# Performance work log

Hardware: AMD Instinct MI355X
Metric: run time of the kernel (lower is better)

The kernel has to match this reference:

```python
import jax, jax.numpy as jnp
import numpy as np

C = 8.0  # RG-LRU temporal-gate constant (Griffin paper, c = 8)


def setup_inputs() -> dict:
    key = jax.random.key(0)
    ks = jax.random.split(key, 4)
    S, B, D = 2048, 8, 2048  # (seq_len, batch, width); batch_first=False layout
    s = 1.0 / np.sqrt(D).astype(np.float32)
    return {
        "x": jax.random.normal(ks[0], (S, B, D), jnp.float32),
        "h0": jnp.zeros((B, D), jnp.float32),
        "W_x": jax.random.normal(ks[1], (D, D), jnp.float32) * s,
        "b_x": jnp.zeros((D,), jnp.float32),
        "W_a": jax.random.normal(ks[2], (D, D), jnp.float32) * s,
        "b_a": jnp.zeros((D,), jnp.float32),
        "a_param": jax.random.uniform(ks[3], (D,), jnp.float32, 0.3, 1.0),
    }


def _rg_lru(x, h0, W_x, b_x, W_a, b_a, a_param):
    # x: (S, B, D) time-major. RG-LRU (Griffin/Hawk), num_heads=1 so the
    # block-diagonal gate projections are plain dense D->D linears.
    S = x.shape[0]
    gate_x = jax.nn.sigmoid(jnp.einsum("sbd,ed->sbe", x, W_x) + b_x)  # input gate
    gate_a = jax.nn.sigmoid(jnp.einsum("sbd,ed->sbe", x, W_a) + b_a)  # recurrence gate
    log_a = -C * gate_a * jax.nn.softplus(a_param)  # (S, B, D), log of decay in (0,1)
    a = jnp.exp(log_a)
    multiplier = jnp.sqrt(1.0 - jnp.exp(2.0 * log_a))  # sqrt(1 - a^2) normalizer
    # Reset at segment start (t == 0): multiplier -> 1, decay -> 0 (cache cleared).
    reset = (jnp.arange(S) == 0)[:, None, None]
    multiplier = jnp.where(reset, 1.0, multiplier)
    a = jnp.where(reset, 0.0, a)
    normed_x = x * gate_x * multiplier  # gated, variance-normalized input

    def step(h, inp):
        a_t, x_t = inp
        h = a_t * h + x_t  # diagonal linear recurrence
        return h, h

    hn, y = jax.lax.scan(step, h0, (a, normed_x))
    return y, hn  # y: (S, B, D) since batch_first=False; hn: (B, D)


def reference(x, h0, W_x, b_x, W_a, b_a, a_param):
    return _rg_lru(x, h0, W_x, b_x, W_a, b_a, a_param)
```

## Files before the change

kernel.cpp:

```cpp
#include <hip/hip_runtime.h>
#include <cstdint>

#define S_LEN 2048
#define B_SZ 8
#define D_DIM 2048
#define M_DIM (S_LEN * B_SZ)
#define CHAINS (B_SZ * D_DIM)
#define BK 64
#define KTILES (D_DIM / BK)

typedef __bf16 bf16;
typedef bf16 bf16x8 __attribute__((ext_vector_type(8)));
typedef bf16 bf16x4 __attribute__((ext_vector_type(4)));
typedef float f32x4 __attribute__((ext_vector_type(4)));

__device__ __forceinline__ void async_copy16(void* lds, const void* g) {
    __builtin_amdgcn_global_load_lds(
        (const __attribute__((address_space(1))) unsigned int*)g,
        (__attribute__((address_space(3))) unsigned int*)lds,
        16, 0, 0);
}

__device__ __forceinline__ unsigned short bf16_bits(float f) {
    bf16 b = (bf16)f;
    return __builtin_bit_cast(unsigned short, b);
}

__global__ void k_convert(const float4* __restrict__ x,
                          const float4* __restrict__ wx,
                          const float4* __restrict__ wa,
                          bf16* __restrict__ xb,
                          bf16* __restrict__ wi) {
    const long NX4 = (long)M_DIM * D_DIM / 4;
    const long NW4 = (long)D_DIM * D_DIM / 4;
    const long total = NX4 + 2 * NW4;
    for (long i = (long)blockIdx.x * blockDim.x + threadIdx.x; i < total;
         i += (long)gridDim.x * blockDim.x) {
        float4 v;
        bf16* dst;
        if (i < NX4) {
            v = x[i];
            dst = xb + 4 * i;
        } else {
            long k = i - NX4;
            const int isA = k >= NW4;
            if (isA) k -= NW4;
            const long e = k >> 9;
            const long col4 = k & 511;
            const long drow = (e >> 4) * 32 + (isA ? 16 : 0) + (e & 15);
            v = (isA ? wa : wx)[k];
            dst = wi + (drow * 512 + col4) * 4;
        }
        bf16x4 o;
        o[0] = (bf16)v.x; o[1] = (bf16)v.y; o[2] = (bf16)v.z; o[3] = (bf16)v.w;
        *reinterpret_cast<bf16x4*>(dst) = o;
    }
}

__global__ void k_cvec(const float* __restrict__ ap, float* __restrict__ cv) {
    int e = blockIdx.x * blockDim.x + threadIdx.x;
    if (e < D_DIM) {
        float v = ap[e];
        cv[e] = -8.0f * log1pf(expf(v));
    }
}

__global__ __launch_bounds__(512, 2) void k_gemm(
    const bf16* __restrict__ xb,
    const bf16* __restrict__ wi,
    const float* __restrict__ bx,
    const float* __restrict__ ba,
    const float* __restrict__ cv,
    unsigned int* __restrict__ pk)
{
    __shared__ __align__(16) char smem[131072];

    const int tid  = threadIdx.x;
    const int lane = tid & 63;
    const int w    = tid >> 6;
    const int wm   = w >> 2;
    const int wn   = w & 3;

    const int orig = blockIdx.x;
    const int wgid = (orig & 7) * 128 + (orig >> 3);
    const int m0 = (wgid & 63) * 256;
    const int e0 = (wgid >> 6) * 256;

    const int srow  = lane >> 3;
    const int swz16 = ((lane & 7) ^ srow) * 16;

    const char* gA = (const char*)xb;
    const char* gB = (const char*)wi;

#define SU_A(buf, kt, u) do {                                                  \
    const int rb_ = (u) * 64 + w * 8;                                          \
    async_copy16(smem + (buf) * 65536 + rb_ * 128,                             \
                 gA + ((long)(m0 + rb_ + srow) * 4096 +                        \
                       (long)(kt) * 128 + swz16));                             \
    } while (0)

#define SU_B(buf, kt, u) do {                                                  \
    const int rb_ = (u) * 64 + w * 8;                                          \
    async_copy16(smem + (buf) * 65536 + 32768 + rb_ * 128,                     \
                 gB + ((long)(e0 + rb_ + srow) * 4096 +                        \
                       (long)(kt) * 128 + swz16));                             \
    } while (0)

    f32x4 acc[8][4];
#pragma unroll
    for (int i = 0; i < 8; ++i)
#pragma unroll
        for (int j = 0; j < 4; ++j) acc[i][j] = (f32x4)(0.0f);

    SU_A(0, 0, 0); SU_A(0, 0, 2);
    SU_B(0, 0, 0); SU_B(0, 0, 1); SU_B(0, 0, 2); SU_B(0, 0, 3);
    SU_A(0, 0, 1); SU_A(0, 0, 3);
    asm volatile("s_waitcnt vmcnt(2)" ::: "memory");
    __builtin_amdgcn_s_barrier();

    const int rL = lane & 15;

    for (int kt = 0; kt < KTILES; ++kt) {
        const int c  = kt & 1;
        const int nb = 1 - c;
        char* sA = smem + c * 65536;
        char* sB = sA + 32768;
        const bool pf = (kt < KTILES - 1);

        bf16x8 af[4], bf[4];

#define LOAD_AF(ihalf, ks) do {                                                \
    _Pragma("unroll")                                                          \
    for (int i_ = 0; i_ < 4; ++i_) {                                           \
        const int r_ = wm * 128 + ((ihalf) * 4 + i_) * 16 + rL;                \
        const int ch_ = (((ks) * 4 + (lane >> 4)) ^ (r_ & 7)) * 16;            \
        af[i_] = *reinterpret_cast<const bf16x8*>(sA + r_ * 128 + ch_);        \
    } } while (0)

#define LOAD_BF(ks) do {                                                       \
    _Pragma("unroll")                                                          \
    for (int j_ = 0; j_ < 4; ++j_) {                                           \
        const int r_ = wn * 64 + j_ * 16 + rL;                                 \
        const int ch_ = (((ks) * 4 + (lane >> 4)) ^ (r_ & 7)) * 16;            \
        bf[j_] = *reinterpret_cast<const bf16x8*>(sB + r_ * 128 + ch_);        \
    } } while (0)

#define MFMA16(ihalf) do {                                                     \
    _Pragma("unroll")                                                          \
    for (int i_ = 0; i_ < 4; ++i_)                                             \
        _Pragma("unroll")                                                      \
        for (int j_ = 0; j_ < 4; ++j_)                                         \
            acc[(ihalf) * 4 + i_][j_] = __builtin_amdgcn_mfma_f32_16x16x32_bf16( \
                af[i_], bf[j_], acc[(ihalf) * 4 + i_][j_], 0, 0, 0);           \
    } while (0)

        LOAD_BF(0); LOAD_AF(0, 0);
        if (pf) { SU_A(nb, kt + 1, 0); SU_A(nb, kt + 1, 2); }
        MFMA16(0);
        if (pf) asm volatile("s_waitcnt vmcnt(2)" ::: "memory");
        else    asm volatile("s_waitcnt vmcnt(0)" ::: "memory");
        __builtin_amdgcn_s_barrier();

        LOAD_AF(1, 0);
        if (pf) { SU_B(nb, kt + 1, 0); SU_B(nb, kt + 1, 1); }
        MFMA16(1);

        LOAD_BF(1); LOAD_AF(0, 1);
        if (pf) { SU_B(nb, kt + 1, 2); SU_B(nb, kt + 1, 3); }
        MFMA16(0);

        LOAD_AF(1, 1);
        if (pf) { SU_A(nb, kt + 1, 1); SU_A(nb, kt + 1, 3); }
        MFMA16(1);

        if (pf) {
            asm volatile("s_waitcnt vmcnt(2)" ::: "memory");
            __builtin_amdgcn_s_barrier();
        }

#undef LOAD_AF
#undef LOAD_BF
#undef MFMA16
    }

#undef SU_A
#undef SU_B

    const int rgrp = lane >> 4;
    const int chb  = (e0 + wn * 64) >> 1;
#pragma unroll
    for (int jj = 0; jj < 2; ++jj) {
        const int ch = chb + jj * 16 + rL;
        const float bxv = bx[ch];
        const float bav = ba[ch];
        const float cvv = cv[ch];
#pragma unroll
        for (int i = 0; i < 8; ++i) {
#pragma unroll
            for (int r = 0; r < 4; ++r) {
                const int m = m0 + wm * 128 + i * 16 + rgrp * 4 + r;
                const float zx = acc[i][2 * jj][r] + bxv;
                const float za = acc[i][2 * jj + 1][r] + bav;
                const float gx = 1.0f / (1.0f + __expf(-zx));
                const float ga = 1.0f / (1.0f + __expf(-za));
                float la = cvv * ga;
                float mult = sqrtf(fmaxf(1.0f - __expf(2.0f * la), 0.0f));
                if (m < B_SZ) { la = -100.0f; mult = 1.0f; }
                const long o = (long)m * D_DIM + ch;
                const float xv = (float)xb[o];
                const float xn = xv * gx * mult;
                const unsigned int u =
                    ((unsigned int)bf16_bits(xn) << 16) | bf16_bits(la);
                pk[o] = u;
            }
        }
    }
}

__global__ __launch_bounds__(64) void k_scan(
    const unsigned int* __restrict__ pk,
    float* __restrict__ y,
    const float* __restrict__ h0,
    float* __restrict__ hn) {
    const int c = blockIdx.x * 64 + threadIdx.x;
    float h = h0[c];

    unsigned int u0[16], u1[16];
#pragma unroll
    for (int j = 0; j < 16; ++j) u0[j] = pk[(long)j * CHAINS + c];

    for (int g = 0; g < 128; g += 2) {
        const long base1 = ((long)(g + 1) * 16) * CHAINS + c;
        if (g + 1 < 128) {
#pragma unroll
            for (int j = 0; j < 16; ++j) u1[j] = pk[base1 + (long)j * CHAINS];
        }
        const long base0 = ((long)g * 16) * CHAINS + c;
#pragma unroll
        for (int j = 0; j < 16; ++j) {
            const unsigned int u = u0[j];
            const float la = __builtin_bit_cast(float, u << 16);
            const float xn = __builtin_bit_cast(float, u & 0xffff0000u);
            h = fmaf(__expf(la), h, xn);
            y[base0 + (long)j * CHAINS] = h;
        }
        const long base2 = ((long)(g + 2) * 16) * CHAINS + c;
        if (g + 2 < 128) {
#pragma unroll
            for (int j = 0; j < 16; ++j) u0[j] = pk[base2 + (long)j * CHAINS];
        }
        if (g + 1 < 128) {
#pragma unroll
            for (int j = 0; j < 16; ++j) {
                const unsigned int u = u1[j];
                const float la = __builtin_bit_cast(float, u << 16);
                const float xn = __builtin_bit_cast(float, u & 0xffff0000u);
                h = fmaf(__expf(la), h, xn);
                y[base1 + (long)j * CHAINS] = h;
            }
        }
    }
    hn[c] = h;
}

extern "C" void kernel_launch(void* const* d_in, const int* in_sizes, int n_in,
                              void* d_out, int out_size, void* d_ws, size_t ws_size,
                              hipStream_t stream) {
    const float* x  = (const float*)d_in[0];
    const float* h0 = (const float*)d_in[1];
    const float* Wx = (const float*)d_in[2];
    const float* bx = (const float*)d_in[3];
    const float* Wa = (const float*)d_in[4];
    const float* ba = (const float*)d_in[5];
    const float* ap = (const float*)d_in[6];
    float* out = (float*)d_out;

    char* ws = (char*)d_ws;
    bf16*  xb = (bf16*)(ws);
    bf16*  wi = (bf16*)(ws + 67108864L);
    float* cv = (float*)(ws + 83886080L);
    unsigned int* pk = (unsigned int*)(ws + 83894272L);

    float* y  = out;
    float* hn = out + (long)M_DIM * D_DIM;

    k_convert<<<dim3(2048), dim3(256), 0, stream>>>(
        (const float4*)x, (const float4*)Wx, (const float4*)Wa, xb, wi);
    k_cvec<<<dim3(8), dim3(256), 0, stream>>>(ap, cv);
    k_gemm<<<dim3((M_DIM / 256) * (2 * D_DIM / 256)), dim3(512), 0, stream>>>(
        xb, wi, bx, ba, cv, pk);
    k_scan<<<dim3(CHAINS / 64), dim3(64), 0, stream>>>(pk, y, h0, hn);
}
```

Measured before the change: 428.2 us.

## Restructure GEMM main loop into quadrant phases with barriers and s_setprio

```diff
diff --git a/kernel.cpp b/kernel.cpp
--- a/kernel.cpp
+++ b/kernel.cpp
@@ -106,16 +106,25 @@
                        (long)(kt) * 128 + swz16));                             \
     } while (0)
 
+#define PHASE_MID() do {                                                       \
+    __builtin_amdgcn_s_barrier();                                              \
+    asm volatile("s_waitcnt lgkmcnt(0)" ::: "memory");                         \
+    __builtin_amdgcn_sched_barrier(0);                                         \
+    __builtin_amdgcn_s_setprio(1); } while (0)
+
+#define PHASE_END() do {                                                       \
+    __builtin_amdgcn_s_setprio(0);                                             \
+    __builtin_amdgcn_s_barrier(); } while (0)
+
     f32x4 acc[8][4];
 #pragma unroll
     for (int i = 0; i < 8; ++i)
 #pragma unroll
         for (int j = 0; j < 4; ++j) acc[i][j] = (f32x4)(0.0f);
 
-    SU_A(0, 0, 0); SU_A(0, 0, 2);
+    SU_A(0, 0, 0); SU_A(0, 0, 1); SU_A(0, 0, 2); SU_A(0, 0, 3);
     SU_B(0, 0, 0); SU_B(0, 0, 1); SU_B(0, 0, 2); SU_B(0, 0, 3);
-    SU_A(0, 0, 1); SU_A(0, 0, 3);
-    asm volatile("s_waitcnt vmcnt(2)" ::: "memory");
+    asm volatile("s_waitcnt vmcnt(0)" ::: "memory");
     __builtin_amdgcn_s_barrier();
 
     const int rL = lane & 15;
@@ -127,64 +136,74 @@
         char* sB = sA + 32768;
         const bool pf = (kt < KTILES - 1);
 
-        bf16x8 af[4], bf[4];
-
-#define LOAD_AF(ihalf, ks) do {                                                \
-    _Pragma("unroll")                                                          \
-    for (int i_ = 0; i_ < 4; ++i_) {                                           \
-        const int r_ = wm * 128 + ((ihalf) * 4 + i_) * 16 + rL;                \
-        const int ch_ = (((ks) * 4 + (lane >> 4)) ^ (r_ & 7)) * 16;            \
-        af[i_] = *reinterpret_cast<const bf16x8*>(sA + r_ * 128 + ch_);        \
-    } } while (0)
-
-#define LOAD_BF(ks) do {                                                       \
-    _Pragma("unroll")                                                          \
-    for (int j_ = 0; j_ < 4; ++j_) {                                           \
-        const int r_ = wn * 64 + j_ * 16 + rL;                                 \
-        const int ch_ = (((ks) * 4 + (lane >> 4)) ^ (r_ & 7)) * 16;            \
-        bf[j_] = *reinterpret_cast<const bf16x8*>(sB + r_ * 128 + ch_);        \
-    } } while (0)
-
-#define MFMA16(ihalf) do {                                                     \
+        bf16x8 a0[8], a1[8], b0[4], b1[4];
+
+#define READ_A(dst, sub) do {                                                  \
     _Pragma("unroll")                                                          \
     for (int i_ = 0; i_ < 4; ++i_)                                             \
         _Pragma("unroll")                                                      \
-        for (int j_ = 0; j_ < 4; ++j_)                                         \
-            acc[(ihalf) * 4 + i_][j_] = __builtin_amdgcn_mfma_f32_16x16x32_bf16( \
-                af[i_], bf[j_], acc[(ihalf) * 4 + i_][j_], 0, 0, 0);           \
+        for (int ks_ = 0; ks_ < 2; ++ks_) {                                    \
+            const int r_ = wm * 128 + (sub) * 64 + i_ * 16 + rL;               \
+            const int ch_ = ((ks_ * 4 + (lane >> 4)) ^ (r_ & 7)) * 16;         \
+            dst[i_ * 2 + ks_] =                                                \
+                *reinterpret_cast<const bf16x8*>(sA + r_ * 128 + ch_);         \
+        } } while (0)
+
+#define READ_B(dst, sub) do {                                                  \
+    _Pragma("unroll")                                                          \
+    for (int j_ = 0; j_ < 2; ++j_)                                             \
+        _Pragma("unroll")                                                      \
+        for (int ks_ = 0; ks_ < 2; ++ks_) {                                    \
+            const int r_ = wn * 64 + (sub) * 32 + j_ * 16 + rL;                \
+            const int ch_ = ((ks_ * 4 + (lane >> 4)) ^ (r_ & 7)) * 16;         \
+            dst[j_ * 2 + ks_] =                                                \
+                *reinterpret_cast<const bf16x8*>(sB + r_ * 128 + ch_);         \
+        } } while (0)
+
+#define MFMAQ(ih, jh, am, bm) do {                                             \
+    _Pragma("unroll")                                                          \
+    for (int i_ = 0; i_ < 4; ++i_)                                             \
+        _Pragma("unroll")                                                      \
+        for (int j_ = 0; j_ < 2; ++j_)                                         \
+            _Pragma("unroll")                                                  \
+            for (int ks_ = 0; ks_ < 2; ++ks_)                                  \
+                acc[(ih) * 4 + i_][(jh) * 2 + j_] =                            \
+                    __builtin_amdgcn_mfma_f32_16x16x32_bf16(                   \
+                        am[i_ * 2 + ks_], bm[j_ * 2 + ks_],                    \
+                        acc[(ih) * 4 + i_][(jh) * 2 + j_], 0, 0, 0);           \
     } while (0)
 
-        LOAD_BF(0); LOAD_AF(0, 0);
-        if (pf) { SU_A(nb, kt + 1, 0); SU_A(nb, kt + 1, 2); }
-        MFMA16(0);
-        if (pf) asm volatile("s_waitcnt vmcnt(2)" ::: "memory");
-        else    asm volatile("s_waitcnt vmcnt(0)" ::: "memory");
+        READ_A(a0, 0); READ_B(b0, 0);
+        if (pf) { SU_A(nb, kt + 1, 0); SU_A(nb, kt + 1, 1);
+                  SU_A(nb, kt + 1, 2); SU_A(nb, kt + 1, 3); }
+        PHASE_MID();
+        MFMAQ(0, 0, a0, b0);
+        PHASE_END();
+
+        READ_B(b1, 1);
+        if (pf) { SU_B(nb, kt + 1, 0); SU_B(nb, kt + 1, 1);
+                  SU_B(nb, kt + 1, 2); SU_B(nb, kt + 1, 3); }
+        PHASE_MID();
+        MFMAQ(0, 1, a0, b1);
+        PHASE_END();
+
+        READ_A(a1, 1);
+        PHASE_MID();
+        MFMAQ(1, 1, a1, b1);
+        MFMAQ(1, 0, a1, b0);
+        __builtin_amdgcn_s_setprio(0);
+        if (pf) asm volatile("s_waitcnt vmcnt(0)" ::: "memory");
         __builtin_amdgcn_s_barrier();
 
-        LOAD_AF(1, 0);
-        if (pf) { SU_B(nb, kt + 1, 0); SU_B(nb, kt + 1, 1); }
-        MFMA16(1);
-
-        LOAD_BF(1); LOAD_AF(0, 1);
-        if (pf) { SU_B(nb, kt + 1, 2); SU_B(nb, kt + 1, 3); }
-        MFMA16(0);
-
-        LOAD_AF(1, 1);
-        if (pf) { SU_A(nb, kt + 1, 1); SU_A(nb, kt + 1, 3); }
-        MFMA16(1);
-
-        if (pf) {
-            asm volatile("s_waitcnt vmcnt(2)" ::: "memory");
-            __builtin_amdgcn_s_barrier();
-        }
-
-#undef LOAD_AF
-#undef LOAD_BF
-#undef MFMA16
+#undef READ_A
+#undef READ_B
+#undef MFMAQ
     }
 
 #undef SU_A
 #undef SU_B
+#undef PHASE_MID
+#undef PHASE_END
 
     const int rgrp = lane >> 4;
     const int chb  = (e0 + wn * 64) >> 1;
```

Result: no change. 427.3 us (-0.2%).

## Pre-swizzle weights into MFMA fragment order and load B directly to registers

Applied to the files above, without the earlier changes.

```diff
diff --git a/kernel.cpp b/kernel.cpp
--- a/kernel.cpp
+++ b/kernel.cpp
@@ -30,30 +30,39 @@
                           const float4* __restrict__ wx,
                           const float4* __restrict__ wa,
                           bf16* __restrict__ xb,
-                          bf16* __restrict__ wi) {
+                          bf16* __restrict__ wsw) {
     const long NX4 = (long)M_DIM * D_DIM / 4;
-    const long NW4 = (long)D_DIM * D_DIM / 4;
-    const long total = NX4 + 2 * NW4;
+    const long NWS = 1048576;
+    const long total = NX4 + NWS;
     for (long i = (long)blockIdx.x * blockDim.x + threadIdx.x; i < total;
          i += (long)gridDim.x * blockDim.x) {
-        float4 v;
-        bf16* dst;
         if (i < NX4) {
-            v = x[i];
-            dst = xb + 4 * i;
+            float4 v = x[i];
+            bf16x4 o;
+            o[0] = (bf16)v.x; o[1] = (bf16)v.y; o[2] = (bf16)v.z; o[3] = (bf16)v.w;
+            *reinterpret_cast<bf16x4*>(xb + 4 * i) = o;
         } else {
-            long k = i - NX4;
-            const int isA = k >= NW4;
-            if (isA) k -= NW4;
-            const long e = k >> 9;
-            const long col4 = k & 511;
-            const long drow = (e >> 4) * 32 + (isA ? 16 : 0) + (e & 15);
-            v = (isA ? wa : wx)[k];
-            dst = wi + (drow * 512 + col4) * 4;
-        }
-        bf16x4 o;
-        o[0] = (bf16)v.x; o[1] = (bf16)v.y; o[2] = (bf16)v.z; o[3] = (bf16)v.w;
-        *reinterpret_cast<bf16x4*>(dst) = o;
+            const long t = i - NX4;
+            const int lane = (int)(t & 63);
+            const long frag = t >> 6;
+            const int ks = (int)(frag & 1);
+            const int cg = (int)((frag >> 1) & 15);
+            const int kt = (int)((frag >> 5) & 31);
+            const int nb = (int)(frag >> 10);
+            const int lr = lane & 15, ch = lane >> 4;
+            const int g  = cg & 1;
+            const int e  = (((nb << 4) | cg) >> 1) * 16 + lr;
+            const int d  = kt * 64 + ks * 32 + ch * 8;
+            const float4* src = (g ? wa : wx) + (long)e * 512 + (d >> 2);
+            const float4 v0 = src[0];
+            const float4 v1 = src[1];
+            bf16x8 o;
+            o[0] = (bf16)v0.x; o[1] = (bf16)v0.y;
+            o[2] = (bf16)v0.z; o[3] = (bf16)v0.w;
+            o[4] = (bf16)v1.x; o[5] = (bf16)v1.y;
+            o[6] = (bf16)v1.z; o[7] = (bf16)v1.w;
+            *reinterpret_cast<bf16x8*>(wsw + t * 8) = o;
+        }
     }
 }
 
@@ -67,13 +76,13 @@
 
 __global__ __launch_bounds__(512, 2) void k_gemm(
     const bf16* __restrict__ xb,
-    const bf16* __restrict__ wi,
+    const bf16* __restrict__ wsw,
     const float* __restrict__ bx,
     const float* __restrict__ ba,
     const float* __restrict__ cv,
     unsigned int* __restrict__ pk)
 {
-    __shared__ __align__(16) char smem[131072];
+    __shared__ __align__(16) char smem[65536];
 
     const int tid  = threadIdx.x;
     const int lane = tid & 63;
@@ -83,51 +92,32 @@
 
     const int orig = blockIdx.x;
     const int wgid = (orig & 7) * 128 + (orig >> 3);
-    const int m0 = (wgid & 63) * 256;
-    const int e0 = (wgid >> 6) * 256;
+    const int m0  = (wgid & 63) * 256;
+    const int nbb = wgid >> 6;
+    const int e0  = nbb * 256;
 
     const int srow  = lane >> 3;
     const int swz16 = ((lane & 7) ^ srow) * 16;
+    const int rL = lane & 15;
 
     const char* gA = (const char*)xb;
-    const char* gB = (const char*)wi;
 
 #define SU_A(buf, kt, u) do {                                                  \
     const int rb_ = (u) * 64 + w * 8;                                          \
-    async_copy16(smem + (buf) * 65536 + rb_ * 128,                             \
+    async_copy16(smem + (buf) * 32768 + rb_ * 128,                             \
                  gA + ((long)(m0 + rb_ + srow) * 4096 +                        \
                        (long)(kt) * 128 + swz16));                             \
     } while (0)
 
-#define SU_B(buf, kt, u) do {                                                  \
-    const int rb_ = (u) * 64 + w * 8;                                          \
-    async_copy16(smem + (buf) * 65536 + 32768 + rb_ * 128,                     \
-                 gB + ((long)(e0 + rb_ + srow) * 4096 +                        \
-                       (long)(kt) * 128 + swz16));                             \
-    } while (0)
-
-    f32x4 acc[8][4];
-#pragma unroll
-    for (int i = 0; i < 8; ++i)
-#pragma unroll
-        for (int j = 0; j < 4; ++j) acc[i][j] = (f32x4)(0.0f);
-
-    SU_A(0, 0, 0); SU_A(0, 0, 2);
-    SU_B(0, 0, 0); SU_B(0, 0, 1); SU_B(0, 0, 2); SU_B(0, 0, 3);
-    SU_A(0, 0, 1); SU_A(0, 0, 3);
-    asm volatile("s_waitcnt vmcnt(2)" ::: "memory");
-    __builtin_amdgcn_s_barrier();
-
-    const int rL = lane & 15;
-
-    for (int kt = 0; kt < KTILES; ++kt) {
-        const int c  = kt & 1;
-        const int nb = 1 - c;
-        char* sA = smem + c * 65536;
-        char* sB = sA + 32768;
-        const bool pf = (kt < KTILES - 1);
-
-        bf16x8 af[4], bf[4];
+#define LOAD_BG(dst, kt) do {                                                  \
+    _Pragma("unroll")                                                          \
+    for (int j_ = 0; j_ < 4; ++j_)                                             \
+        _Pragma("unroll")                                                      \
+        for (int ks_ = 0; ks_ < 2; ++ks_)                                      \
+            dst[j_ * 2 + ks_] = *reinterpret_cast<const bf16x8*>(              \
+                wsw + ((((long)nbb * 32 + (kt)) * 32) +                        \
+                       (wn * 4 + j_) * 2 + ks_) * 512 + lane * 8);             \
+    } while (0)
 
 #define LOAD_AF(ihalf, ks) do {                                                \
     _Pragma("unroll")                                                          \
@@ -137,54 +127,62 @@
         af[i_] = *reinterpret_cast<const bf16x8*>(sA + r_ * 128 + ch_);        \
     } } while (0)
 
-#define LOAD_BF(ks) do {                                                       \
-    _Pragma("unroll")                                                          \
-    for (int j_ = 0; j_ < 4; ++j_) {                                           \
-        const int r_ = wn * 64 + j_ * 16 + rL;                                 \
-        const int ch_ = (((ks) * 4 + (lane >> 4)) ^ (r_ & 7)) * 16;            \
-        bf[j_] = *reinterpret_cast<const bf16x8*>(sB + r_ * 128 + ch_);        \
-    } } while (0)
-
-#define MFMA16(ihalf) do {                                                     \
+#define MFMA16(ihalf, ks, bm) do {                                             \
     _Pragma("unroll")                                                          \
     for (int i_ = 0; i_ < 4; ++i_)                                             \
         _Pragma("unroll")                                                      \
         for (int j_ = 0; j_ < 4; ++j_)                                         \
-            acc[(ihalf) * 4 + i_][j_] = __builtin_amdgcn_mfma_f32_16x16x32_bf16( \
-                af[i_], bf[j_], acc[(ihalf) * 4 + i_][j_], 0, 0, 0);           \
-    } while (0)
-
-        LOAD_BF(0); LOAD_AF(0, 0);
-        if (pf) { SU_A(nb, kt + 1, 0); SU_A(nb, kt + 1, 2); }
-        MFMA16(0);
-        if (pf) asm volatile("s_waitcnt vmcnt(2)" ::: "memory");
-        else    asm volatile("s_waitcnt vmcnt(0)" ::: "memory");
-        __builtin_amdgcn_s_barrier();
-
-        LOAD_AF(1, 0);
-        if (pf) { SU_B(nb, kt + 1, 0); SU_B(nb, kt + 1, 1); }
-        MFMA16(1);
-
-        LOAD_BF(1); LOAD_AF(0, 1);
-        if (pf) { SU_B(nb, kt + 1, 2); SU_B(nb, kt + 1, 3); }
-        MFMA16(0);
-
-        LOAD_AF(1, 1);
-        if (pf) { SU_A(nb, kt + 1, 1); SU_A(nb, kt + 1, 3); }
-        MFMA16(1);
-
-        if (pf) {
-            asm volatile("s_waitcnt vmcnt(2)" ::: "memory");
-            __builtin_amdgcn_s_barrier();
-        }
-
+            acc[(ihalf) * 4 + i_][j_] =                                        \
+                __builtin_amdgcn_mfma_f32_16x16x32_bf16(                       \
+                    af[i_], bm[j_ * 2 + (ks)],                                 \
+                    acc[(ihalf) * 4 + i_][j_], 0, 0, 0);                       \
+    } while (0)
+
+    f32x4 acc[8][4];
+#pragma unroll
+    for (int i = 0; i < 8; ++i)
+#pragma unroll
+        for (int j = 0; j < 4; ++j) acc[i][j] = (f32x4)(0.0f);
+
+    bf16x8 b0[8], b1[8];
+
+    SU_A(0, 0, 0); SU_A(0, 0, 1); SU_A(0, 0, 2); SU_A(0, 0, 3);
+    asm volatile("" ::: "memory");
+    LOAD_BG(b0, 0);
+    asm volatile("s_waitcnt vmcnt(8)" ::: "memory");
+    __builtin_amdgcn_s_barrier();
+
+#define TILE(kt, bcur, bnxt) do {                                              \
+    const int c_ = (kt) & 1;                                                   \
+    const char* sA = smem + c_ * 32768;                                        \
+    const bool pf_ = (kt) < KTILES - 1;                                        \
+    bf16x8 af[4];                                                              \
+    if (pf_) {                                                                 \
+        SU_A(1 - c_, (kt) + 1, 0); SU_A(1 - c_, (kt) + 1, 1);                  \
+        SU_A(1 - c_, (kt) + 1, 2); SU_A(1 - c_, (kt) + 1, 3);                  \
+        asm volatile("" ::: "memory");              \
+        LOAD_BG(bnxt, (kt) + 1);                                               \
+    }                                                                          \
+    LOAD_AF(0, 0); MFMA16(0, 0, bcur);                                         \
+    LOAD_AF(1, 0); MFMA16(1, 0, bcur);                                         \
+    LOAD_AF(0, 1); MFMA16(0, 1, bcur);                                         \
+    LOAD_AF(1, 1); MFMA16(1, 1, bcur);                                         \
+    if (pf_) {                                                                 \
+        asm volatile("s_waitcnt vmcnt(8)" ::: "memory");                       \
+        __builtin_amdgcn_s_barrier();                                          \
+    }                                                                          \
+    } while (0)
+
+    for (int it = 0; it < KTILES / 2; ++it) {
+        TILE(2 * it, b0, b1);
+        TILE(2 * it + 1, b1, b0);
+    }
+
+#undef TILE
+#undef SU_A
+#undef LOAD_BG
 #undef LOAD_AF
-#undef LOAD_BF
 #undef MFMA16
-    }
-
-#undef SU_A
-#undef SU_B
 
     const int rgrp = lane >> 4;
     const int chb  = (e0 + wn * 64) >> 1;
@@ -276,18 +274,18 @@
     float* out = (float*)d_out;
 
     char* ws = (char*)d_ws;
-    bf16*  xb = (bf16*)(ws);
-    bf16*  wi = (bf16*)(ws + 67108864L);
-    float* cv = (float*)(ws + 83886080L);
+    bf16*  xb  = (bf16*)(ws);
+    bf16*  wsw = (bf16*)(ws + 67108864L);
+    float* cv  = (float*)(ws + 83886080L);
     unsigned int* pk = (unsigned int*)(ws + 83894272L);
 
     float* y  = out;
     float* hn = out + (long)M_DIM * D_DIM;
 
     k_convert<<<dim3(2048), dim3(256), 0, stream>>>(
-        (const float4*)x, (const float4*)Wx, (const float4*)Wa, xb, wi);
+        (const float4*)x, (const float4*)Wx, (const float4*)Wa, xb, wsw);
     k_cvec<<<dim3(8), dim3(256), 0, stream>>>(ap, cv);
     k_gemm<<<dim3((M_DIM / 256) * (2 * D_DIM / 256)), dim3(512), 0, stream>>>(
-        xb, wi, bx, ba, cv, pk);
+        xb, wsw, bx, ba, cv, pk);
     k_scan<<<dim3(CHAINS / 64), dim3(64), 0, stream>>>(pk, y, h0, hn);
 }
```

New measurement: 438.3 us. 1.02x slower.
